# Kernel optimization log

Hardware: AMD Instinct MI355X
Metric: run time of the kernel (lower is better)

The kernel has to match this reference:

```python
import jax, jax.numpy as jnp
import numpy as np

DIM = 256        # word / relation / entity-type embedding dim
STATEDIM = 256   # agent state dim
VOCAB = 100000
REL_COUNT = 25
T = 128          # sentence length


def _lstm(wvs, Wih, Whh, bih, bhh, reverse):
    # PyTorch LSTMCell gate order: i, f, g, o
    def step(carry, x):
        h, c = carry
        g = x @ Wih.T + bih + h @ Whh.T + bhh
        i, f, gg, o = jnp.split(g, 4)
        c = jax.nn.sigmoid(f) * c + jax.nn.sigmoid(i) * jnp.tanh(gg)
        h = jax.nn.sigmoid(o) * jnp.tanh(c)
        return (h, c), h
    init = (jnp.zeros((DIM,), jnp.float32), jnp.zeros((DIM,), jnp.float32))
    _, hs = jax.lax.scan(step, init, wvs, reverse=reverse)
    return hs


def setup_inputs() -> dict:
    key = jax.random.key(0)
    ks = jax.random.split(key, 32)
    def p(i, shape, scale=0.05):
        return (jax.random.normal(ks[i], shape) * scale).astype(jnp.float32)
    return {
        "text": jax.random.randint(ks[0], (T,), 0, VOCAB, dtype=jnp.int32),
        "wordvector": p(1, (VOCAB, DIM)),
        "relvec": p(2, (REL_COUNT + 1, DIM)),
        "entvec": p(3, (7, DIM)),
        "WihL": p(4, (4 * DIM, DIM)), "WhhL": p(5, (4 * DIM, DIM)),
        "bihL": p(6, (4 * DIM,)), "bhhL": p(7, (4 * DIM,)),
        "WihR": p(8, (4 * DIM, DIM)), "WhhR": p(9, (4 * DIM, DIM)),
        "bihR": p(10, (4 * DIM,)), "bhhR": p(11, (4 * DIM,)),
        "Wt": p(12, (STATEDIM, 3 * DIM + STATEDIM)), "bt": p(13, (STATEDIM,)),
        "Wp": p(14, (REL_COUNT + 1, STATEDIM)), "bp": p(15, (REL_COUNT + 1,)),
        "Wb": p(16, (STATEDIM, 3 * DIM + 2 * STATEDIM)), "bb": p(17, (STATEDIM,)),
        "Wpl": p(18, (REL_COUNT, 7, STATEDIM)), "bpl": p(19, (REL_COUNT, 7)),
        "Wtt": p(20, (STATEDIM, STATEDIM)), "btt": p(21, (STATEDIM,)),
        "Wtb": p(22, (STATEDIM, STATEDIM)), "btb": p(23, (STATEDIM,)),
        "Wbt": p(24, (STATEDIM, STATEDIM)), "bbt": p(25, (STATEDIM,)),
    }


def reference(text, wordvector, relvec, entvec, WihL, WhhL, bihL, bhhL,
              WihR, WhhR, bihR, bhhR, Wt, bt, Wp, bp, Wb, bb, Wpl, bpl,
              Wtt, btt, Wtb, btb, Wbt, bbt):
    # mode = "test_NER": deterministic argmax sampling, dropout disabled.
    wvs = wordvector[text]                               # [T, DIM]
    front = _lstm(wvs, WihL, WhhL, bihL, bhhL, False)    # [T, DIM]
    back = _lstm(wvs, WihR, WhhR, bihR, bhhR, True)      # [T, DIM]
    wordin = jnp.concatenate([front, back], axis=1)      # [T, 2*DIM]

    def bot_rollout(rel_idx, target, memb0):
        Wr, br = Wpl[rel_idx], bpl[rel_idx]              # per-relation head
        def stepb(carry, w):
            memb, ab = carry
            inpb = jnp.concatenate([w, entvec[ab], memb, target])
            outb = jnp.tanh(inpb @ Wb.T + bb)            # dropout off (test)
            probb = jax.nn.softmax(outb @ Wr.T + br)
            ab2 = jnp.argmax(probb).astype(jnp.int32)
            return (outb, ab2), (ab2, probb[ab2])
        (membf, _), (acts, aps) = jax.lax.scan(
            stepb, (memb0, jnp.zeros((), jnp.int32)), wordin)
        return membf, acts, aps

    def top_step(carry, w):
        mem, rel_action = carry
        inp = jnp.concatenate([w, relvec[rel_action], mem])
        outp = jnp.tanh(inp @ Wt.T + bt)                 # dropout off (test)
        prob = jax.nn.softmax(outp @ Wp.T + bp)
        action = jnp.argmax(prob).astype(jnp.int32)
        actprob = prob[action]
        do_ner = action > 0
        rel_next = jnp.where(do_ner, action, rel_action)
        rel_idx = jnp.maximum(action, 1) - 1
        target = outp @ Wtt.T + btt
        memb0 = outp @ Wtb.T + btb
        membf, acts, aps = bot_rollout(rel_idx, target, memb0)
        mem_after = membf @ Wbt.T + bbt
        mem_next = jnp.where(do_ner, mem_after, outp)
        acts = jnp.where(do_ner, acts, 0)
        aps = jnp.where(do_ner, aps, 0.0)
        return (mem_next, rel_next), (action, actprob, acts, aps)

    init = (jnp.zeros((STATEDIM,), jnp.float32), jnp.zeros((), jnp.int32))
    _, (top_actions, top_actprobs, bot_actions, bot_actprobs) = jax.lax.scan(
        top_step, init, wordin)
    # bot rows where no NER sub-rollout fired are zero-filled (orig: empty lists)
    return top_actions, top_actprobs, bot_actions, bot_actprobs
```

## Files before the change

kernel.cpp:

```cpp
#include <hip/hip_runtime.h>
#include <float.h>

constexpr int SEQ  = 128;
constexpr int D    = 256;
constexpr int G    = 1024;
constexpr int NREL = 26;
constexpr int NENT = 7;

typedef float v2f __attribute__((ext_vector_type(2)));
typedef float v4f __attribute__((ext_vector_type(4)));

__global__ void k_trans(const float* __restrict__ in, float* __restrict__ out,
                        int rows, int cols, int in_stride, int in_off)
{
    int idx = blockIdx.x * 256 + threadIdx.x;
    if (idx >= rows * cols) return;
    int i = idx % rows;
    int k = idx / rows;
    out[idx] = in[(size_t)i * in_stride + in_off + k];
}

__global__ __launch_bounds__(1024) void k_xg(
    const int* __restrict__ text, const float* __restrict__ wv,
    const float* __restrict__ Wih, const float* __restrict__ bih,
    const float* __restrict__ bhh, float* __restrict__ xg)
{
    int t = blockIdx.x, j = threadIdx.x;
    const float* x  = wv + (size_t)text[t] * D;
    const float* wr = Wih + (size_t)j * D;
    float acc = bih[j] + bhh[j];
    for (int k = 0; k < D; ++k) acc += x[k] * wr[k];
    xg[t * G + j] = acc;
}

__global__ __launch_bounds__(1024) void k_lstm(
    const float* __restrict__ xgF, const float* __restrict__ xgB,
    const float* __restrict__ WHTF, const float* __restrict__ WHTB,
    float* __restrict__ wordin)
{
    int dir = blockIdx.x;
    const float* xg  = dir ? xgB  : xgF;
    const float* WHT = dir ? WHTB : WHTF;
    __shared__ float h[D], c[D], g[G];
    int j = threadIdx.x;
    if (j < D) { h[j] = 0.f; c[j] = 0.f; }
    __syncthreads();
    for (int s = 0; s < SEQ; ++s) {
        int t = dir ? (SEQ - 1 - s) : s;
        float acc = xg[t * G + j];
        for (int k = 0; k < D; ++k) acc += WHT[k * G + j] * h[k];
        g[j] = acc;
        __syncthreads();
        if (j < D) {
            float si = 1.f / (1.f + expf(-g[j]));
            float sf = 1.f / (1.f + expf(-g[D + j]));
            float gg = tanhf(g[2 * D + j]);
            float so = 1.f / (1.f + expf(-g[3 * D + j]));
            float cn = sf * c[j] + si * gg;
            float hn = so * tanhf(cn);
            c[j] = cn; h[j] = hn;
            wordin[t * (2 * D) + dir * D + j] = hn;
        }
        __syncthreads();
    }
}

__global__ __launch_bounds__(256) void k_prep2(
    const float* __restrict__ wordin,
    const float* __restrict__ WTWT, const float* __restrict__ WBWT,
    const float* __restrict__ WTRT, const float* __restrict__ WBET,
    const float* __restrict__ relvec, const float* __restrict__ entvec,
    const float* __restrict__ btv, const float* __restrict__ bbv,
    float* __restrict__ TW, float* __restrict__ BW,
    float* __restrict__ RV, float* __restrict__ EV)
{
    int b = blockIdx.x, i = threadIdx.x;
    if (b < SEQ) {
        const float* w = wordin + b * (2 * D);
        float a1 = btv[i], a2 = bbv[i];
        for (int j = 0; j < 2 * D; ++j) {
            float wv = w[j];
            a1 += wv * WTWT[j * D + i];
            a2 += wv * WBWT[j * D + i];
        }
        TW[b * D + i] = a1;
        BW[b * D + i] = a2;
    } else if (b < SEQ + NREL) {
        int r = b - SEQ;
        const float* x = relvec + r * D;
        float a = 0.f;
        for (int k = 0; k < D; ++k) a += x[k] * WTRT[k * D + i];
        RV[r * D + i] = a;
    } else {
        int e = b - SEQ - NREL;
        const float* x = entvec + e * D;
        float a = 0.f;
        for (int k = 0; k < D; ++k) a += x[k] * WBET[k * D + i];
        EV[e * D + i] = a;
    }
}

__global__ __launch_bounds__(256) void k_m1(
    const float* __restrict__ WBGT, const float* __restrict__ Wtt,
    float* __restrict__ M1T)
{
    int j = blockIdx.x, i = threadIdx.x;
    float a = 0.f;
    for (int k = 0; k < D; ++k) a = fmaf(WBGT[k * D + i], Wtt[k * D + j], a);
    M1T[j * D + i] = a;
}

__global__ __launch_bounds__(256) void k_c1(
    const float* __restrict__ WBGT, const float* __restrict__ btt,
    float* __restrict__ c1)
{
    int i = threadIdx.x;
    float a = 0.f;
    for (int k = 0; k < D; ++k) a = fmaf(WBGT[k * D + i], btt[k], a);
    c1[i] = a;
}

__global__ __launch_bounds__(256) void k_packAr(
    const float* __restrict__ Wb, float* __restrict__ WREG)
{
    int e = blockIdx.x * 256 + threadIdx.x;
    if (e >= 512 * 56) return;
    int tid = e / 56, q = e % 56;
    int h = tid >> 8, i = tid & 255;
    WREG[e] = Wb[(size_t)i * (5 * D) + 3 * D + h * 128 + q];
}

__global__ __launch_bounds__(256) void k_packAl(
    const float* __restrict__ Wb, float* __restrict__ WLDS)
{
    int f = blockIdx.x * 256 + threadIdx.x;
    if (f >= 512 * 72) return;
    int f4 = f >> 2, c = f & 3;
    int l = f4 & 63, rest = f4 >> 6;
    int j = rest % 18, w = rest / 18;
    int tid = w * 64 + l;
    int h = tid >> 8, i = tid & 255;
    WLDS[f] = Wb[(size_t)i * (5 * D) + 3 * D + h * 128 + 56 + 4 * j + c];
}

__device__ inline float mv_half(const float* __restrict__ Wcol,
                                const float* __restrict__ x)
{
    float a0 = 0.f, a1 = 0.f, a2 = 0.f, a3 = 0.f;
    #pragma unroll
    for (int kk = 0; kk < 128; kk += 4) {
        a0 = fmaf(Wcol[(kk + 0) * D], x[kk + 0], a0);
        a1 = fmaf(Wcol[(kk + 1) * D], x[kk + 1], a1);
        a2 = fmaf(Wcol[(kk + 2) * D], x[kk + 2], a2);
        a3 = fmaf(Wcol[(kk + 3) * D], x[kk + 3], a3);
    }
    return (a0 + a1) + (a2 + a3);
}

template<int W>
__device__ inline void grp_smax(float lv, int n, int lane, int& am, float& pm)
{
    float mx = lv;
    #pragma unroll
    for (int off = W / 2; off; off >>= 1) mx = fmaxf(mx, __shfl_xor(mx, off));
    float e  = (lane < n) ? expf(lv - mx) : 0.f;
    float se = e;
    #pragma unroll
    for (int off = W / 2; off; off >>= 1) se += __shfl_xor(se, off);
    float p  = (lane < n) ? (e / se) : -1.f;
    float q  = p;
    #pragma unroll
    for (int off = W / 2; off; off >>= 1) q = fmaxf(q, __shfl_xor(q, off));
    unsigned long long mask = __ballot(p == q);
    am = __ffsll((long long)mask) - 1;
    pm = q;
}

#define FMA_AB(Wv, Xv)                                                        \
    { v4f xx_ = (Xv);                                                         \
      A0 = __builtin_elementwise_fma((v2f){(Wv).x, (Wv).y},                   \
                                     (v2f){xx_.x, xx_.y}, A0);                \
      A1 = __builtin_elementwise_fma((v2f){(Wv).z, (Wv).w},                   \
                                     (v2f){xx_.z, xx_.w}, A1); }
#define FMA_CD(Wv, Xv)                                                        \
    { v4f xx_ = (Xv);                                                         \
      A2 = __builtin_elementwise_fma((v2f){(Wv).x, (Wv).y},                   \
                                     (v2f){xx_.x, xx_.y}, A2);                \
      A3 = __builtin_elementwise_fma((v2f){(Wv).z, (Wv).w},                   \
                                     (v2f){xx_.z, xx_.w}, A3); }

#define LC(j0)                                                                \
    { v4f la = wbase[(j0 + 0) * 64], lb = wbase[(j0 + 1) * 64],               \
          lc = wbase[(j0 + 2) * 64], ld = wbase[(j0 + 3) * 64];               \
      FMA_AB(la, xb[14 + j0 + 0]) FMA_CD(lb, xb[14 + j0 + 1])                 \
      FMA_AB(lc, xb[14 + j0 + 2]) FMA_CD(ld, xb[14 + j0 + 3])                 \
      __builtin_amdgcn_sched_barrier(0); }

__global__ __launch_bounds__(512)
void k_mainA(
    const float* __restrict__ TW,   const float* __restrict__ BW,
    const float* __restrict__ RV,   const float* __restrict__ EV,
    const float* __restrict__ WTMT, const float* __restrict__ WTBT,
    const float* __restrict__ WBTT, const float* __restrict__ M1T,
    const float* __restrict__ c1v,  const float* __restrict__ WREG,
    const float* __restrict__ WLDS,
    const float* __restrict__ Wp,   const float* __restrict__ bp,
    const float* __restrict__ Wpl,  const float* __restrict__ bpl,
    const float* __restrict__ btb,  const float* __restrict__ bbt,
    float* __restrict__ out)
{
    const int tid  = threadIdx.x;
    const int lane = tid & 63;
    const int wv8  = tid >> 6;
    const int lwv  = wv8 & 3;
    const int h    = tid >> 8;
    const int i    = tid & 255;
    const bool lower = (tid < 256);

    __shared__ __align__(16) float wlds[512 * 72];
    __shared__ __align__(16) float xbuf[2][D];
    __shared__ __align__(16) float psA[2][D];
    __shared__ __align__(16) float mem[D], outv[D];
    __shared__ __align__(16) float WrSh[NENT * D];
    __shared__ float lpart[4][32];
    __shared__ float brSh[8];

    {
        const float4* g4 = reinterpret_cast<const float4*>(WLDS);
        float4* w4 = reinterpret_cast<float4*>(wlds);
        #pragma unroll
        for (int it = 0; it < 18; ++it) w4[tid + it * 512] = g4[tid + it * 512];
    }

    const v4f* r4 = reinterpret_cast<const v4f*>(WREG) + tid * 14;
    v4f wr0 = r4[0],   wr1 = r4[1],   wr2 = r4[2],   wr3 = r4[3];
    v4f wr4 = r4[4],   wr5 = r4[5],   wr6 = r4[6],   wr7 = r4[7];
    v4f wr8 = r4[8],   wr9 = r4[9],   wr10 = r4[10], wr11 = r4[11];
    v4f wr12 = r4[12], wr13 = r4[13];

    float ev0 = EV[0 * D + i], ev1 = EV[1 * D + i], ev2 = EV[2 * D + i],
          ev3 = EV[3 * D + i], ev4 = EV[4 * D + i], ev5 = EV[5 * D + i],
          ev6 = EV[6 * D + i];
    if (lower) mem[i] = 0.f;
    __syncthreads();

    const v4f* wbase =
        reinterpret_cast<const v4f*>(wlds) + (size_t)wv8 * (18 * 64) + lane;

    const float* WTMh = WTMT + (size_t)h * 128 * D + i;
    const float* WTBh = WTBT + (size_t)h * 128 * D + i;
    const float* WBTh = WBTT + (size_t)h * 128 * D + i;
    const float* M1h  = M1T  + (size_t)h * 128 * D + i;

    int rel = 0;

    #pragma unroll 1
    for (int t = 0; t < SEQ; ++t) {
        psA[h][i] = mv_half(WTMh, mem + h * 128);
        __syncthreads();
        if (lower) {
            float tot = psA[0][i] + psA[1][i] +
                        TW[t * D + i] + RV[rel * D + i];
            float outp = tanhf(tot);
            outv[i] = outp;
            #pragma unroll 2
            for (int r = 0; r < NREL; ++r) {
                float pp = outp * Wp[r * D + i];
                #pragma unroll
                for (int off = 32; off; off >>= 1) pp += __shfl_xor(pp, off);
                if (lane == 0) lpart[lwv][r] = pp;
            }
        }
        __syncthreads();
        float lv = -FLT_MAX;
        if (lane < NREL)
            lv = lpart[0][lane] + lpart[1][lane] + lpart[2][lane] +
                 lpart[3][lane] + bp[lane];
        int am; float pm;
        grp_smax<32>(lv, NREL, lane, am, pm);
        if (tid == 0) { out[t] = (float)am; out[SEQ + t] = pm; }
        const int action = am;

        if (action > 0) {
            rel = action;
            psA[h][i] = mv_half(WTBh, outv + h * 128);
            const size_t wb0 = (size_t)(action - 1) * NENT * D;
            for (int k = tid; k < NENT * D; k += 512) WrSh[k] = Wpl[wb0 + k];
            if (tid < NENT) brSh[tid] = bpl[(action - 1) * NENT + tid];
            __syncthreads();
            if (lower) xbuf[0][i] = psA[0][i] + psA[1][i] + btb[i];
            __syncthreads();
            psA[h][i] = mv_half(M1h, outv + h * 128);
            __syncthreads();
            float btm = 0.f, bwc = 0.f;
            if (lower) {
                btm = psA[0][i] + psA[1][i] + c1v[i];
                bwc = BW[i];
            }
            __syncthreads();

            int p = 0, ab = 0;
            #pragma unroll 1
            for (int s = 0; s < SEQ; ++s) {
                const v4f* xb = reinterpret_cast<const v4f*>(xbuf[p] + h * 128);
                v2f A0 = {0.f, 0.f}, A1 = {0.f, 0.f},
                    A2 = {0.f, 0.f}, A3 = {0.f, 0.f};
                FMA_AB(wr0,  xb[0])  FMA_CD(wr1,  xb[1])
                FMA_AB(wr2,  xb[2])  FMA_CD(wr3,  xb[3])
                __builtin_amdgcn_sched_barrier(0);
                FMA_AB(wr4,  xb[4])  FMA_CD(wr5,  xb[5])
                FMA_AB(wr6,  xb[6])  FMA_CD(wr7,  xb[7])
                __builtin_amdgcn_sched_barrier(0);
                FMA_AB(wr8,  xb[8])  FMA_CD(wr9,  xb[9])
                FMA_AB(wr10, xb[10]) FMA_CD(wr11, xb[11])
                __builtin_amdgcn_sched_barrier(0);
                FMA_AB(wr12, xb[12]) FMA_CD(wr13, xb[13])
                __builtin_amdgcn_sched_barrier(0);
                LC(0) LC(4) LC(8) LC(12)
                { v4f la = wbase[16 * 64], lb = wbase[17 * 64];
                  FMA_AB(la, xb[30]) FMA_CD(lb, xb[31]) }
                v2f AS = (A0 + A1) + (A2 + A3);
                float ms = AS.x + AS.y;
                psA[h][i] = ms;
                __syncthreads();
                if (lower) {
                    float ev = (ab == 0) ? ev0 : (ab == 1) ? ev1 :
                               (ab == 2) ? ev2 : (ab == 3) ? ev3 :
                               (ab == 4) ? ev4 : (ab == 5) ? ev5 : ev6;
                    float tot = ms + psA[1][i] + bwc + ev + btm;
                    float ob = tanhf(tot);
                    xbuf[p ^ 1][i] = ob;
                    #pragma unroll
                    for (int r = 0; r < NENT; ++r) {
                        float pp = ob * WrSh[r * D + i];
                        #pragma unroll
                        for (int off = 32; off; off >>= 1)
                            pp += __shfl_xor(pp, off);
                        if (lane == 0) lpart[lwv][r] = pp;
                    }
                    int sn = (s + 1 < SEQ) ? s + 1 : s;
                    bwc = BW[sn * D + i];
                }
                __syncthreads();
                float lv2 = -FLT_MAX;
                if (lane < NENT)
                    lv2 = lpart[0][lane] + lpart[1][lane] + lpart[2][lane] +
                          lpart[3][lane] + brSh[lane];
                int am2; float pm2;
                grp_smax<8>(lv2, NENT, lane, am2, pm2);
                if (tid == 0) {
                    out[2 * SEQ + t * SEQ + s] = (float)am2;
                    out[2 * SEQ + SEQ * SEQ + t * SEQ + s] = pm2;
                }
                ab = am2;
                p ^= 1;
            }
            psA[h][i] = mv_half(WBTh, xbuf[p] + h * 128);
            __syncthreads();
            if (lower) mem[i] = psA[0][i] + psA[1][i] + bbt[i];
            __syncthreads();
        } else {
            if (lower) mem[i] = outv[i];
            if (tid < SEQ) {
                out[2 * SEQ + t * SEQ + tid] = 0.f;
                out[2 * SEQ + SEQ * SEQ + t * SEQ + tid] = 0.f;
            }
            __syncthreads();
        }
    }
}

extern "C" void kernel_launch(void* const* d_in, const int* in_sizes, int n_in,
                              void* d_out, int out_size, void* d_ws, size_t ws_size,
                              hipStream_t stream)
{
    (void)in_sizes; (void)n_in; (void)out_size; (void)ws_size;
    const int*   text       = (const int*)  d_in[0];
    const float* wordvector = (const float*)d_in[1];
    const float* relvec     = (const float*)d_in[2];
    const float* entvec     = (const float*)d_in[3];
    const float* WihL = (const float*)d_in[4];  const float* WhhL = (const float*)d_in[5];
    const float* bihL = (const float*)d_in[6];  const float* bhhL = (const float*)d_in[7];
    const float* WihR = (const float*)d_in[8];  const float* WhhR = (const float*)d_in[9];
    const float* bihR = (const float*)d_in[10]; const float* bhhR = (const float*)d_in[11];
    const float* Wt   = (const float*)d_in[12]; const float* bt   = (const float*)d_in[13];
    const float* Wp   = (const float*)d_in[14]; const float* bp   = (const float*)d_in[15];
    const float* Wb   = (const float*)d_in[16]; const float* bb   = (const float*)d_in[17];
    const float* Wpl  = (const float*)d_in[18]; const float* bpl  = (const float*)d_in[19];
    const float* Wtt  = (const float*)d_in[20]; const float* btt  = (const float*)d_in[21];
    const float* Wtb  = (const float*)d_in[22]; const float* btb  = (const float*)d_in[23];
    const float* Wbt  = (const float*)d_in[24]; const float* bbt  = (const float*)d_in[25];

    float* ws = (float*)d_ws;
    size_t o = 0;
    auto take = [&](size_t n) { float* p = ws + o; o += n; return p; };
    float* XGF    = take(SEQ * G);
    float* XGB    = take(SEQ * G);
    float* WHLT   = take(D * G);
    float* WHRT   = take(D * G);
    float* WORDIN = take(SEQ * 2 * D);
    float* TW     = take(SEQ * D);
    float* BW     = take(SEQ * D);
    float* RVb    = take(NREL * D);
    float* EVb    = take(NENT * D);
    float* WTWT   = take(2 * D * D);
    float* WTRT   = take(D * D);
    float* WTMT   = take(D * D);
    float* WBWT   = take(2 * D * D);
    float* WBET   = take(D * D);
    float* WBGT   = take(D * D);
    float* WTBT   = take(D * D);
    float* WBTT   = take(D * D);
    float* M1T    = take(D * D);
    float* C1     = take(D);
    float* WREG   = take(512 * 56);
    float* WLDS   = take(512 * 72);

    auto tr = [&](const float* in, float* outp, int rows, int cols, int stride, int off) {
        int n = rows * cols;
        k_trans<<<(n + 255) / 256, 256, 0, stream>>>(in, outp, rows, cols, stride, off);
    };
    tr(WhhL, WHLT, G, D, D, 0);
    tr(WhhR, WHRT, G, D, D, 0);
    tr(Wt,  WTWT, D, 2 * D, G, 0);
    tr(Wt,  WTRT, D, D, G, 512);
    tr(Wt,  WTMT, D, D, G, 768);
    tr(Wb,  WBWT, D, 2 * D, 5 * D, 0);
    tr(Wb,  WBET, D, D, 5 * D, 512);
    tr(Wb,  WBGT, D, D, 5 * D, 1024);
    tr(Wtb, WTBT, D, D, D, 0);
    tr(Wbt, WBTT, D, D, D, 0);

    k_m1<<<D, D, 0, stream>>>(WBGT, Wtt, M1T);
    k_c1<<<1, D, 0, stream>>>(WBGT, btt, C1);
    k_packAr<<<(512 * 56 + 255) / 256, 256, 0, stream>>>(Wb, WREG);
    k_packAl<<<(512 * 72 + 255) / 256, 256, 0, stream>>>(Wb, WLDS);

    k_xg<<<SEQ, 1024, 0, stream>>>(text, wordvector, WihL, bihL, bhhL, XGF);
    k_xg<<<SEQ, 1024, 0, stream>>>(text, wordvector, WihR, bihR, bhhR, XGB);
    k_lstm<<<2, 1024, 0, stream>>>(XGF, XGB, WHLT, WHRT, WORDIN);
    k_prep2<<<SEQ + NREL + NENT, 256, 0, stream>>>(WORDIN, WTWT, WBWT, WTRT, WBET,
                                                   relvec, entvec, bt, bb,
                                                   TW, BW, RVb, EVb);
    k_mainA<<<1, 512, 0, stream>>>(TW, BW, RVb, EVb, WTMT, WTBT, WBTT, M1T, C1,
                                   WREG, WLDS, Wp, bp, Wpl, bpl, btb, bbt,
                                   (float*)d_out);
}
```

Before: 61.71 ms.

## Stream bottom-rollout weights from global per step instead of pinning in registers

The 56 register-resident weight columns per thread in the inner bottom rollout are replaced by coalesced global (L2/L1-cached) loads issued at the start of each step, overlapping with the LDS-part FMAs which now run first. The seven entity-vector registers and select chain are replaced by a per-step EV load indexed by the previous action, and the next-step bias loads move after the argmax. This frees VGPRs (the mv_half unroll is also reduced) at the cost of reissuing 14 vector global loads every inner step on a single-block serial kernel.

```diff
diff --git a/kernel.cpp b/kernel.cpp
--- a/kernel.cpp
+++ b/kernel.cpp
@@ -120,17 +120,18 @@
     c1[i] = a;
 }
 
-__global__ __launch_bounds__(256) void k_packAr(
-    const float* __restrict__ Wb, float* __restrict__ WREG)
-{
-    int e = blockIdx.x * 256 + threadIdx.x;
-    if (e >= 512 * 56) return;
-    int tid = e / 56, q = e % 56;
+__global__ __launch_bounds__(256) void k_packBg(
+    const float* __restrict__ Wb, float* __restrict__ WGL)
+{
+    int f = blockIdx.x * 256 + threadIdx.x;
+    if (f >= 512 * 56) return;
+    int f4 = f >> 2, c = f & 3;
+    int tid = f4 & 511, n = f4 >> 9;
     int h = tid >> 8, i = tid & 255;
-    WREG[e] = Wb[(size_t)i * (5 * D) + 3 * D + h * 128 + q];
-}
-
-__global__ __launch_bounds__(256) void k_packAl(
+    WGL[f] = Wb[(size_t)i * (5 * D) + 3 * D + h * 128 + 4 * n + c];
+}
+
+__global__ __launch_bounds__(256) void k_packBl(
     const float* __restrict__ Wb, float* __restrict__ WLDS)
 {
     int f = blockIdx.x * 256 + threadIdx.x;
@@ -147,7 +148,7 @@
                                 const float* __restrict__ x)
 {
     float a0 = 0.f, a1 = 0.f, a2 = 0.f, a3 = 0.f;
-    #pragma unroll
+    #pragma unroll 8
     for (int kk = 0; kk < 128; kk += 4) {
         a0 = fmaf(Wcol[(kk + 0) * D], x[kk + 0], a0);
         a1 = fmaf(Wcol[(kk + 1) * D], x[kk + 1], a1);
@@ -197,13 +198,13 @@
       __builtin_amdgcn_sched_barrier(0); }
 
 __global__ __launch_bounds__(512)
-void k_mainA(
+void k_mainB(
     const float* __restrict__ TW,   const float* __restrict__ BW,
     const float* __restrict__ RV,   const float* __restrict__ EV,
     const float* __restrict__ WTMT, const float* __restrict__ WTBT,
     const float* __restrict__ WBTT, const float* __restrict__ M1T,
-    const float* __restrict__ c1v,  const float* __restrict__ WREG,
-    const float* __restrict__ WLDS,
+    const float* __restrict__ c1v,  const float* __restrict__ WLDS,
+    const float* __restrict__ WGL,
     const float* __restrict__ Wp,   const float* __restrict__ bp,
     const float* __restrict__ Wpl,  const float* __restrict__ bpl,
     const float* __restrict__ btb,  const float* __restrict__ bbt,
@@ -231,21 +232,12 @@
         #pragma unroll
         for (int it = 0; it < 18; ++it) w4[tid + it * 512] = g4[tid + it * 512];
     }
-
-    const v4f* r4 = reinterpret_cast<const v4f*>(WREG) + tid * 14;
-    v4f wr0 = r4[0],   wr1 = r4[1],   wr2 = r4[2],   wr3 = r4[3];
-    v4f wr4 = r4[4],   wr5 = r4[5],   wr6 = r4[6],   wr7 = r4[7];
-    v4f wr8 = r4[8],   wr9 = r4[9],   wr10 = r4[10], wr11 = r4[11];
-    v4f wr12 = r4[12], wr13 = r4[13];
-
-    float ev0 = EV[0 * D + i], ev1 = EV[1 * D + i], ev2 = EV[2 * D + i],
-          ev3 = EV[3 * D + i], ev4 = EV[4 * D + i], ev5 = EV[5 * D + i],
-          ev6 = EV[6 * D + i];
     if (lower) mem[i] = 0.f;
     __syncthreads();
 
     const v4f* wbase =
         reinterpret_cast<const v4f*>(wlds) + (size_t)wv8 * (18 * 64) + lane;
+    const v4f* gl = reinterpret_cast<const v4f*>(WGL) + tid;
 
     const float* WTMh = WTMT + (size_t)h * 128 * D + i;
     const float* WTBh = WTBT + (size_t)h * 128 * D + i;
@@ -292,42 +284,51 @@
             __syncthreads();
             psA[h][i] = mv_half(M1h, outv + h * 128);
             __syncthreads();
-            float btm = 0.f, bwc = 0.f;
+            float btm = 0.f, bwc = 0.f, evn = 0.f;
             if (lower) {
                 btm = psA[0][i] + psA[1][i] + c1v[i];
                 bwc = BW[i];
+                evn = EV[i];
             }
             __syncthreads();
 
             int p = 0, ab = 0;
             #pragma unroll 1
             for (int s = 0; s < SEQ; ++s) {
+                const v4f* glv = gl;
+                asm volatile("" : "+v"(glv));
+                v4f g0  = glv[0 * 512],  g1  = glv[1 * 512],
+                    g2  = glv[2 * 512],  g3  = glv[3 * 512],
+                    g4  = glv[4 * 512],  g5  = glv[5 * 512],
+                    g6  = glv[6 * 512],  g7  = glv[7 * 512],
+                    g8  = glv[8 * 512],  g9  = glv[9 * 512],
+                    g10 = glv[10 * 512], g11 = glv[11 * 512],
+                    g12 = glv[12 * 512], g13 = glv[13 * 512];
+                __builtin_amdgcn_sched_barrier(0);
+
                 const v4f* xb = reinterpret_cast<const v4f*>(xbuf[p] + h * 128);
                 v2f A0 = {0.f, 0.f}, A1 = {0.f, 0.f},
                     A2 = {0.f, 0.f}, A3 = {0.f, 0.f};
-                FMA_AB(wr0,  xb[0])  FMA_CD(wr1,  xb[1])
-                FMA_AB(wr2,  xb[2])  FMA_CD(wr3,  xb[3])
-                __builtin_amdgcn_sched_barrier(0);
-                FMA_AB(wr4,  xb[4])  FMA_CD(wr5,  xb[5])
-                FMA_AB(wr6,  xb[6])  FMA_CD(wr7,  xb[7])
-                __builtin_amdgcn_sched_barrier(0);
-                FMA_AB(wr8,  xb[8])  FMA_CD(wr9,  xb[9])
-                FMA_AB(wr10, xb[10]) FMA_CD(wr11, xb[11])
-                __builtin_amdgcn_sched_barrier(0);
-                FMA_AB(wr12, xb[12]) FMA_CD(wr13, xb[13])
-                __builtin_amdgcn_sched_barrier(0);
                 LC(0) LC(4) LC(8) LC(12)
                 { v4f la = wbase[16 * 64], lb = wbase[17 * 64];
                   FMA_AB(la, xb[30]) FMA_CD(lb, xb[31]) }
+                __builtin_amdgcn_sched_barrier(0);
+                FMA_AB(g0,  xb[0])  FMA_CD(g1,  xb[1])
+                FMA_AB(g2,  xb[2])  FMA_CD(g3,  xb[3])
+                __builtin_amdgcn_sched_barrier(0);
+                FMA_AB(g4,  xb[4])  FMA_CD(g5,  xb[5])
+                FMA_AB(g6,  xb[6])  FMA_CD(g7,  xb[7])
+                __builtin_amdgcn_sched_barrier(0);
+                FMA_AB(g8,  xb[8])  FMA_CD(g9,  xb[9])
+                FMA_AB(g10, xb[10]) FMA_CD(g11, xb[11])
+                __builtin_amdgcn_sched_barrier(0);
+                FMA_AB(g12, xb[12]) FMA_CD(g13, xb[13])
                 v2f AS = (A0 + A1) + (A2 + A3);
                 float ms = AS.x + AS.y;
                 psA[h][i] = ms;
                 __syncthreads();
                 if (lower) {
-                    float ev = (ab == 0) ? ev0 : (ab == 1) ? ev1 :
-                               (ab == 2) ? ev2 : (ab == 3) ? ev3 :
-                               (ab == 4) ? ev4 : (ab == 5) ? ev5 : ev6;
-                    float tot = ms + psA[1][i] + bwc + ev + btm;
+                    float tot = ms + psA[1][i] + bwc + evn + btm;
                     float ob = tanhf(tot);
                     xbuf[p ^ 1][i] = ob;
                     #pragma unroll
@@ -338,8 +339,6 @@
                             pp += __shfl_xor(pp, off);
                         if (lane == 0) lpart[lwv][r] = pp;
                     }
-                    int sn = (s + 1 < SEQ) ? s + 1 : s;
-                    bwc = BW[sn * D + i];
                 }
                 __syncthreads();
                 float lv2 = -FLT_MAX;
@@ -353,6 +352,11 @@
                     out[2 * SEQ + SEQ * SEQ + t * SEQ + s] = pm2;
                 }
                 ab = am2;
+                if (lower) {
+                    int sn = (s + 1 < SEQ) ? s + 1 : s;
+                    bwc = BW[sn * D + i];
+                    evn = EV[ab * D + i];
+                }
                 p ^= 1;
             }
             psA[h][i] = mv_half(WBTh, xbuf[p] + h * 128);
@@ -413,8 +417,8 @@
     float* WBTT   = take(D * D);
     float* M1T    = take(D * D);
     float* C1     = take(D);
-    float* WREG   = take(512 * 56);
     float* WLDS   = take(512 * 72);
+    float* WGL    = take(512 * 56);
 
     auto tr = [&](const float* in, float* outp, int rows, int cols, int stride, int off) {
         int n = rows * cols;
@@ -433,8 +437,8 @@
 
     k_m1<<<D, D, 0, stream>>>(WBGT, Wtt, M1T);
     k_c1<<<1, D, 0, stream>>>(WBGT, btt, C1);
-    k_packAr<<<(512 * 56 + 255) / 256, 256, 0, stream>>>(Wb, WREG);
-    k_packAl<<<(512 * 72 + 255) / 256, 256, 0, stream>>>(Wb, WLDS);
+    k_packBl<<<(512 * 72 + 255) / 256, 256, 0, stream>>>(Wb, WLDS);
+    k_packBg<<<(512 * 56 + 255) / 256, 256, 0, stream>>>(Wb, WGL);
 
     k_xg<<<SEQ, 1024, 0, stream>>>(text, wordvector, WihL, bihL, bhhL, XGF);
     k_xg<<<SEQ, 1024, 0, stream>>>(text, wordvector, WihR, bihR, bhhR, XGB);
@@ -442,7 +446,7 @@
     k_prep2<<<SEQ + NREL + NENT, 256, 0, stream>>>(WORDIN, WTWT, WBWT, WTRT, WBET,
                                                    relvec, entvec, bt, bb,
                                                    TW, BW, RVb, EVb);
-    k_mainA<<<1, 512, 0, stream>>>(TW, BW, RVb, EVb, WTMT, WTBT, WBTT, M1T, C1,
-                                   WREG, WLDS, Wp, bp, Wpl, bpl, btb, bbt,
+    k_mainB<<<1, 512, 0, stream>>>(TW, BW, RVb, EVb, WTMT, WTBT, WBTT, M1T, C1,
+                                   WLDS, WGL, Wp, bp, Wpl, bpl, btb, bbt,
                                    (float*)d_out);
 }
```

Measured after the change: 63.10 ms. +2.3%, slower.
